# Kernel tuning notes

Measured on AMD Instinct MI355X. Metric: run time of the kernel, lower is better.

Reference implementation:

```python
import jax, jax.numpy as jnp
import numpy as np

HEADS, DIM_HEAD, LANDMARKS, PINV_ITERS = 8, 64, 256, 6
CONV_K = 33  # nystrom residual depthwise conv kernel


def _pinv(x, iters):
    # Moore-Penrose iterative pseudo-inverse (lucidrains nystrom-attention)
    ax = jnp.abs(x)
    denom = ax.sum(-1).max() * ax.sum(-2).max()
    z = jnp.swapaxes(x, -1, -2) / denom
    I = jnp.eye(x.shape[-1], dtype=x.dtype)
    for _ in range(iters):
        xz = x @ z
        z = 0.25 * z @ (13.0 * I - xz @ (15.0 * I - xz @ (7.0 * I - xz)))
    return z


def _nystrom(x, qkv_w, out_w, out_b, conv_w):
    b, n, _ = x.shape
    m = LANDMARKS
    pad = (m - n % m) % m
    x = jnp.pad(x, ((0, 0), (pad, 0), (0, 0)))  # pad at front, as in reference impl
    npad = n + pad
    qkv = x @ qkv_w  # (b, npad, 3*h*dh), no bias
    q, k, v = jnp.split(qkv, 3, axis=-1)
    heads = lambda t: t.reshape(b, npad, HEADS, DIM_HEAD).transpose(0, 2, 1, 3)  # bhnd
    q, k, v = heads(q), heads(k), heads(v)
    q = q * (DIM_HEAD ** -0.5)
    l = npad // m
    q_l = q.reshape(b, HEADS, m, l, DIM_HEAD).mean(3)  # (b,h,m,dh) landmarks
    k_l = k.reshape(b, HEADS, m, l, DIM_HEAD).mean(3)
    attn1 = jax.nn.softmax(jnp.einsum('bhid,bhjd->bhij', q, k_l), -1)    # (b,h,npad,m)
    attn2 = jax.nn.softmax(jnp.einsum('bhid,bhjd->bhij', q_l, k_l), -1)  # (b,h,m,m)
    attn3 = jax.nn.softmax(jnp.einsum('bhid,bhjd->bhij', q_l, k), -1)    # (b,h,m,npad)
    out = (attn1 @ _pinv(attn2, PINV_ITERS)) @ (attn3 @ v)               # (b,h,npad,dh)
    # residual depthwise conv along sequence dim (groups=heads)
    res = jax.lax.conv_general_dilated(
        v, conv_w, (1, 1), ((CONV_K // 2, CONV_K // 2), (0, 0)),
        dimension_numbers=('NCHW', 'OIHW', 'NCHW'), feature_group_count=HEADS)
    out = out + res
    out = out.transpose(0, 2, 1, 3).reshape(b, npad, HEADS * DIM_HEAD)
    out = out @ out_w + out_b
    return out[:, -n:]  # drop front padding


def setup_inputs() -> dict:
    key = jax.random.key(0)
    ks = jax.random.split(key, 12)
    N, D, E, WP = 30000, 1024, 480000, 256
    inner = HEADS * DIM_HEAD
    s = lambda k, shape, fan: jax.random.normal(k, shape, jnp.float32) * (fan ** -0.5)
    return {
        'dense': jax.random.normal(ks[0], (1, N, D), jnp.float32),
        'edge_index': jax.random.randint(ks[1], (2, E), 0, N),
        'adj_vals': jax.random.uniform(ks[2], (E,), jnp.float32),
        'qkv_w': s(ks[3], (D, 3 * inner), D),
        'out_w': s(ks[4], (inner, D), inner),
        'out_b': jnp.zeros((D,), jnp.float32),
        'conv_w': s(ks[5], (HEADS, 1, CONV_K, 1), CONV_K),
        'wq_w': s(ks[6], (D, WP), D),
        'wq_b': jnp.zeros((WP,), jnp.float32),
        'wk_w': s(ks[7], (D, WP), D),
        'wk_b': jnp.zeros((WP,), jnp.float32),
        'wv_w': s(ks[8], (D, D), D),
        'wv_b': jnp.zeros((D,), jnp.float32),
    }


def reference(dense, edge_index, adj_vals, qkv_w, out_w, out_b, conv_w,
              wq_w, wq_b, wk_w, wk_b, wv_w, wv_b):
    n = dense.shape[1]
    enc = _nystrom(dense, qkv_w, out_w, out_b, conv_w)  # (1, n, D)
    encoder_output = enc[0] + dense                     # (1, n, D), broadcast as in torch
    x = encoder_output[0]                               # (n, D)
    # CustomAttention: per-edge dot-product scores
    q = x @ wq_w + wq_b                                 # (n, 256)
    k = x @ wk_w + wk_b
    scores = jnp.sum(q[edge_index[0]] * k[edge_index[1]], axis=-1) / jnp.sqrt(jnp.float32(q.shape[-1]))
    # NeighborAggregator: elementwise sparse mult by adjacency values, row-sum, global softmax
    A_raw = jax.ops.segment_sum(scores * adj_vals, edge_index[0], num_segments=n)  # (n,)
    norm_alpha = jax.nn.softmax(A_raw)
    value = dense @ wv_w + wv_b                         # (1, n, D)
    xl = norm_alpha[:, None] * value                    # (1, n, D)
    sw = jax.nn.sigmoid(-xl) ** 2
    xo = xl * 2.0 * sw + 2.0 * encoder_output * (1.0 - sw)
    return xo, A_raw
```

## Files before the change

kernel.cpp:

```cpp
#include <hip/hip_runtime.h>

#define NSEQ   30000
#define NPAD   30208
#define FPAD   208
#define DMODEL 1024
#define NHEAD  8
#define DHEAD  64
#define LM     256
#define LCHUNK 118
#define INNER  512
#define NCHUNK 59

typedef long long ll;
typedef unsigned short us;
typedef unsigned int uint32;
typedef __attribute__((ext_vector_type(8))) __bf16 bf16x8;
typedef __attribute__((ext_vector_type(4))) float f32x4;

__device__ __forceinline__ float b2f(us u) {
    union { unsigned int i; float f; } x; x.i = ((unsigned int)u) << 16; return x.f;
}
__device__ __forceinline__ us f2b(float f) {
    union { float f; unsigned int i; } x; x.f = f;
    unsigned int r = x.i + 0x7fffu + ((x.i >> 16) & 1u);
    return (us)(r >> 16);
}
__device__ __forceinline__ void gload16(const us* g, us* l) {
    __builtin_amdgcn_global_load_lds(
        (__attribute__((address_space(1))) void*)(const_cast<us*>(g)),
        (__attribute__((address_space(3))) void*)l, 16, 0, 0);
}

template<int EPI>
__global__ __launch_bounds__(256)
void bgemm(const us* __restrict__ A, const us* __restrict__ Bt,
           float* __restrict__ C, us* __restrict__ C2,
           const float* __restrict__ bias, const float* __restrict__ addp,
           int Mm, int Nn, int Kk, int lda, int ldb, int ldc, int ldadd,
           int Mstore, int Nstore, int rSub)
{
    __shared__ us As[2][128 * 32];
    __shared__ us Bs[2][128 * 32];

    int nwg = gridDim.x * gridDim.y;
    int orig = blockIdx.y * gridDim.x + blockIdx.x;
    int qd = nwg >> 3, rm = nwg & 7;
    int xcd = orig & 7, off = orig >> 3;
    int swz = (xcd < rm ? xcd * (qd + 1) : rm * (qd + 1) + (xcd - rm) * qd) + off;
    int by = swz / gridDim.x, bx = swz - by * gridDim.x;
    int m0 = by * 128, n0 = bx * 128;

    int tid = threadIdx.x, w = tid >> 6, lane = tid & 63;
    int wr = w >> 1, wc = w & 1;
    int nkt = Kk >> 5;

    int q0 = w * 128;
    int qa0 = q0 + lane, qa1 = q0 + 64 + lane;
    int r0s = qa0 >> 2, c0s = (qa0 & 3) ^ ((r0s >> 1) & 3);
    int r1s = qa1 >> 2, c1s = (qa1 & 3) ^ ((r1s >> 1) & 3);
    int ar0 = m0 + r0s; if (ar0 > Mm - 1) ar0 = Mm - 1;
    int ar1 = m0 + r1s; if (ar1 > Mm - 1) ar1 = Mm - 1;
    int br0 = n0 + r0s; if (br0 > Nn - 1) br0 = Nn - 1;
    int br1 = n0 + r1s; if (br1 > Nn - 1) br1 = Nn - 1;
    const us* pa0 = A + (ll)ar0 * lda + c0s * 8;
    const us* pa1 = A + (ll)ar1 * lda + c1s * 8;
    const us* pb0 = Bt + (ll)br0 * ldb + c0s * 8;
    const us* pb1 = Bt + (ll)br1 * ldb + c1s * 8;
    int la0o = q0 * 8, la1o = (q0 + 64) * 8;

    int l15 = lane & 15, l4 = lane >> 4;
    int aoff[4], boff[4];
#pragma unroll
    for (int f = 0; f < 4; f++) {
        int row = wr * 64 + f * 16 + l15;
        aoff[f] = row * 32 + ((l4 ^ ((row >> 1) & 3)) << 3);
        int col = wc * 64 + f * 16 + l15;
        boff[f] = col * 32 + ((l4 ^ ((col >> 1) & 3)) << 3);
    }

    f32x4 acc[4][4];
#pragma unroll
    for (int i = 0; i < 4; i++)
#pragma unroll
        for (int j = 0; j < 4; j++) acc[i][j] = (f32x4){0.f, 0.f, 0.f, 0.f};

    auto stage = [&](int buf, int kt) {
        int k0 = kt << 5;
        gload16(pa0 + k0, &As[buf][la0o]);
        gload16(pa1 + k0, &As[buf][la1o]);
        gload16(pb0 + k0, &Bs[buf][la0o]);
        gload16(pb1 + k0, &Bs[buf][la1o]);
    };

    stage(0, 0);
    for (int kt = 0; kt < nkt; ++kt) {
        int cur = kt & 1;
        if (kt + 1 < nkt) {
            stage(cur ^ 1, kt + 1);
            asm volatile("s_waitcnt vmcnt(4)" ::: "memory");
        } else {
            asm volatile("s_waitcnt vmcnt(0)" ::: "memory");
        }
        __builtin_amdgcn_s_barrier();
        asm volatile("" ::: "memory");
        bf16x8 af[4], bfr[4];
#pragma unroll
        for (int f = 0; f < 4; f++) af[f] = *(const bf16x8*)&As[cur][aoff[f]];
#pragma unroll
        for (int f = 0; f < 4; f++) bfr[f] = *(const bf16x8*)&Bs[cur][boff[f]];
#pragma unroll
        for (int i = 0; i < 4; i++)
#pragma unroll
            for (int j = 0; j < 4; j++)
                acc[i][j] = __builtin_amdgcn_mfma_f32_16x16x32_bf16(af[i], bfr[j], acc[i][j], 0, 0, 0);
        asm volatile("" ::: "memory");
        __builtin_amdgcn_s_barrier();
        asm volatile("" ::: "memory");
    }

#pragma unroll
    for (int fm = 0; fm < 4; fm++) {
        int rb = m0 + wr * 64 + fm * 16 + l4 * 4;
#pragma unroll
        for (int fn = 0; fn < 4; fn++) {
            int c = n0 + wc * 64 + fn * 16 + l15;
            if (c >= Nstore) continue;
#pragma unroll
            for (int i = 0; i < 4; i++) {
                int r = rb + i - rSub;
                if (r < 0 || r >= Mstore) continue;
                float v = acc[fm][fn][i];
                if (EPI == 3) {
                    int part = c >> 9, hh = (c >> 6) & 7, dd = c & 63;
                    float o = (part == 0) ? v * 0.125f : v;
                    C2[((ll)(part * 8 + hh) * NPAD + r) * 64 + dd] = f2b(o);
                } else if (EPI == 10) {
                    C2[(ll)r * ldc + c] = f2b(v + bias[c]);
                } else if (EPI == 12) {
                    C2[(ll)r * ldc + c] = f2b(v + bias[c] + addp[(ll)r * ldadd + c]);
                }
            }
        }
    }
}

__global__ __launch_bounds__(512)
void mega1(const us* __restrict__ XN, us* __restrict__ ZN, us* __restrict__ ZT,
           us* __restrict__ ZN2, us* __restrict__ ZT2,
           us* __restrict__ Y, us* __restrict__ W1T, us* __restrict__ W2T,
           us* __restrict__ W3T,
           const us* __restrict__ QLB, const us* __restrict__ Kh,
           const us* __restrict__ VT, us* __restrict__ KVPb, float* __restrict__ ZP,
           const us* __restrict__ Vh, const float* __restrict__ cw,
           us* __restrict__ ATTP,
           const us* __restrict__ DENSEP, const us* __restrict__ WVT,
           const float* __restrict__ wvb, us* __restrict__ VALB)
{
    __shared__ us LDSu[24576];
    int b = blockIdx.x;
    int tid = threadIdx.x, w = tid >> 6, lane = tid & 63;
    int l15 = lane & 15, l4 = lane >> 4;

    if (b < 8) {
        __builtin_amdgcn_s_setprio(1);
        ll hb = (ll)b << 16;
        int wr = w >> 2, wc = w & 3;
        int sra = tid >> 2, sca = ((tid & 3) ^ ((sra >> 1) & 3)) * 8;
        int q1 = tid + 512;
        int srb1 = q1 >> 2, scb1 = ((q1 & 3) ^ ((srb1 >> 1) & 3)) * 8;
        int aoff[4], boff[4];
#pragma unroll
        for (int f = 0; f < 4; f++) {
            int row = wr * 64 + f * 16 + l15;
            aoff[f] = row * 32 + ((l4 ^ ((row >> 1) & 3)) << 3);
            int col = wc * 64 + f * 16 + l15;
            boff[f] = 4096 + col * 32 + ((l4 ^ ((col >> 1) & 3)) << 3);
        }
        f32x4 acc[4][4];
        auto gemmS = [&](const us* Ah, const us* Bt) {
#pragma unroll
            for (int i = 0; i < 4; i++)
#pragma unroll
                for (int j = 0; j < 4; j++) acc[i][j] = (f32x4){0.f, 0.f, 0.f, 0.f};
            const us* pa  = Ah + (ll)sra * 256 + sca;
            const us* pb0 = Bt + (ll)sra * 256 + sca;
            const us* pb1 = Bt + (ll)srb1 * 256 + scb1;
            auto stg = [&](int buf, int kt) {
                int k0 = kt << 5;
                gload16(pa + k0, &LDSu[buf + tid * 8]);
                gload16(pb0 + k0, &LDSu[buf + 4096 + tid * 8]);
                gload16(pb1 + k0, &LDSu[buf + 8192 + tid * 8]);
            };
            stg(0, 0);
            for (int kt = 0; kt < 8; ++kt) {
                int buf = (kt & 1) * 12288;
                if (kt < 7) {
                    stg(buf ^ 12288, kt + 1);
                    asm volatile("s_waitcnt vmcnt(3)" ::: "memory");
                } else {
                    asm volatile("s_waitcnt vmcnt(0)" ::: "memory");
                }
                __builtin_amdgcn_s_barrier();
                asm volatile("" ::: "memory");
                bf16x8 af[4], bfr[4];
#pragma unroll
                for (int f = 0; f < 4; f++) af[f] = *(const bf16x8*)&LDSu[buf + aoff[f]];
#pragma unroll
                for (int f = 0; f < 4; f++) bfr[f] = *(const bf16x8*)&LDSu[buf + boff[f]];
#pragma unroll
                for (int i = 0; i < 4; i++)
#pragma unroll
                    for (int j = 0; j < 4; j++)
                        acc[i][j] = __builtin_amdgcn_mfma_f32_16x16x32_bf16(af[i], bfr[j], acc[i][j], 0, 0, 0);
                asm volatile("" ::: "memory");
                __builtin_amdgcn_s_barrier();
                asm volatile("" ::: "memory");
            }
        };

        us* znc = ZN; us* ztc = ZT; us* znn = ZN2; us* ztn = ZT2;
        for (int it = 0; it < 6; ++it) {
#pragma unroll
            for (int hf = 0; hf < 2; ++hf) {
                gemmS(XN + hb + hf * 32768, ztc + hb);
#pragma unroll
                for (int fm = 0; fm < 4; fm++) {
                    int rb = hf * 128 + wr * 64 + fm * 16 + l4 * 4;
#pragma unroll
                    for (int fn = 0; fn < 4; fn++) {
                        int c = wc * 64 + fn * 16 + l15;
                        ushort4 u;
#pragma unroll
                        for (int i = 0; i < 4; i++) {
                            float v = acc[fm][fn][i];
                            Y[hb + (ll)(rb + i) * 256 + c] = f2b(v);
                            ((us*)&u)[i] = f2b(((rb + i == c) ? 7.0f : 0.0f) - v);
                        }
                        *(ushort4*)&W1T[hb + (ll)c * 256 + rb] = u;
                    }
                }
            }
            __syncthreads();
#pragma unroll
            for (int hf = 0; hf < 2; ++hf) {
                gemmS(Y + hb + hf * 32768, W1T + hb);
#pragma unroll
                for (int fm = 0; fm < 4; fm++) {
                    int rb = hf * 128 + wr * 64 + fm * 16 + l4 * 4;
#pragma unroll
                    for (int fn = 0; fn < 4; fn++) {
                        int c = wc * 64 + fn * 16 + l15;
                        ushort4 u;
#pragma unroll
                        for (int i = 0; i < 4; i++)
                            ((us*)&u)[i] = f2b(((rb + i == c) ? 15.0f : 0.0f) - acc[fm][fn][i]);
                        *(ushort4*)&W2T[hb + (ll)c * 256 + rb] = u;
                    }
                }
            }
            __syncthreads();
#pragma unroll
            for (int hf = 0; hf < 2; ++hf) {
                gemmS(Y + hb + hf * 32768, W2T + hb);
#pragma unroll
                for (int fm = 0; fm < 4; fm++) {
                    int rb = hf * 128 + wr * 64 + fm * 16 + l4 * 4;
#pragma unroll
                    for (int fn = 0; fn < 4; fn++) {
                        int c = wc * 64 + fn * 16 + l15;
                        ushort4 u;
#pragma unroll
                        for (int i = 0; i < 4; i++)
                            ((us*)&u)[i] = f2b(((rb + i == c) ? 13.0f : 0.0f) - acc[fm][fn][i]);
                        *(ushort4*)&W3T[hb + (ll)c * 256 + rb] = u;
                    }
                }
            }
            __syncthreads();
#pragma unroll
            for (int hf = 0; hf < 2; ++hf) {
                gemmS(znc + hb + hf * 32768, W3T + hb);
#pragma unroll
                for (int fm = 0; fm < 4; fm++) {
                    int rb = hf * 128 + wr * 64 + fm * 16 + l4 * 4;
#pragma unroll
                    for (int fn = 0; fn < 4; fn++) {
                        int c = wc * 64 + fn * 16 + l15;
                        ushort4 u;
#pragma unroll
                        for (int i = 0; i < 4; i++) {
                            us q = f2b(0.25f * acc[fm][fn][i]);
                            znn[hb + (ll)(rb + i) * 256 + c] = q;
                            ((us*)&u)[i] = q;
                        }
                        *(ushort4*)&ztn[hb + (ll)c * 256 + rb] = u;
                    }
                }
            }
            __syncthreads();
            us* tp;
            tp = znc; znc = znn; znn = tp;
            tp = ztc; ztc = ztn; ztn = tp;
        }
    } else if (b < 480) {
        if (w >= 4) return;
        int idx = b - 8;
        int h = idx & 7, chunk = idx >> 3;
        int c0 = chunk * 512;
        const us* QLh = QLB + (ll)h * 16384;
        const us* Khh = Kh + (ll)h * NPAD * 64;
        const us* VTh = VT + (ll)h * 64 * NPAD;
        us* P = &LDSu[w * 4096];

        bf16x8 aq[4][2];
#pragma unroll
        for (int fm = 0; fm < 4; fm++)
#pragma unroll
            for (int ks = 0; ks < 2; ks++)
                aq[fm][ks] = *(const bf16x8*)&QLh[(w * 64 + fm * 16 + l15) * 64 + l4 * 8 + ks * 32];

        f32x4 acc2[4][4];
        float zacc[4][4];
#pragma unroll
        for (int a = 0; a < 4; a++)
#pragma unroll
            for (int bb = 0; bb < 4; bb++) { acc2[a][bb] = (f32x4){0.f,0.f,0.f,0.f}; zacc[a][bb] = 0.f; }

        for (int sub = 0; sub < 8; ++sub) {
            int s0 = c0 + sub * 64;
            f32x4 s[4][4];
#pragma unroll
            for (int a = 0; a < 4; a++)
#pragma unroll
                for (int bb = 0; bb < 4; bb++) s[a][bb] = (f32x4){0.f,0.f,0.f,0.f};
#pragma unroll
            for (int ks = 0; ks < 2; ks++) {
                bf16x8 bk[4];
#pragma unroll
                for (int fn = 0; fn < 4; fn++)
                    bk[fn] = *(const bf16x8*)&Khh[(ll)(s0 + fn * 16 + l15) * 64 + l4 * 8 + ks * 32];
#pragma unroll
                for (int fm = 0; fm < 4; fm++)
#pragma unroll
                    for (int fn = 0; fn < 4; fn++)
                        s[fm][fn] = __builtin_amdgcn_mfma_f32_16x16x32_bf16(aq[fm][ks], bk[fn], s[fm][fn], 0, 0, 0);
            }
#pragma unroll
            for (int fm = 0; fm < 4; fm++)
#pragma unroll
                for (int i = 0; i < 4; i++) {
                    int row = fm * 16 + l4 * 4 + i;
#pragma unroll
                    for (int fn = 0; fn < 4; fn++) {
                        float e = __expf(s[fm][fn][i]);
                        zacc[fm][i] += e;
                        int col = fn * 16 + l15;
                        P[row * 64 + (((col >> 3) ^ (row & 7)) << 3) + (col & 7)] = f2b(e);
                    }
                }
#pragma unroll
            for (int ks = 0; ks < 2; ks++) {
                bf16x8 ap[4], bv[4];
#pragma unroll
                for (int fm = 0; fm < 4; fm++) {
                    int row = fm * 16 + l15;
                    int ch = (l4 + ks * 4) ^ (row & 7);
                    ap[fm] = *(const bf16x8*)&P[row * 64 + ch * 8];
                }
#pragma unroll
                for (int fn = 0; fn < 4; fn++)
                    bv[fn] = *(const bf16x8*)&VTh[(ll)(fn * 16 + l15) * NPAD + s0 + l4 * 8 + ks * 32];
#pragma unroll
                for (int fm = 0; fm < 4; fm++)
#pragma unroll
                    for (int fn = 0; fn < 4; fn++)
                        acc2[fm][fn] = __builtin_amdgcn_mfma_f32_16x16x32_bf16(ap[fm], bv[fn], acc2[fm][fn], 0, 0, 0);
            }
        }
        us* KP = KVPb + ((ll)h * NCHUNK + chunk) * 16384;
#pragma unroll
        for (int fm = 0; fm < 4; fm++)
#pragma unroll
            for (int fn = 0; fn < 4; fn++)
#pragma unroll
                for (int i = 0; i < 4; i++)
                    KP[(w * 64 + fm * 16 + l4 * 4 + i) * 64 + fn * 16 + l15] = f2b(acc2[fm][fn][i]);
#pragma unroll
        for (int fm = 0; fm < 4; fm++)
#pragma unroll
            for (int i = 0; i < 4; i++) {
                float zz = zacc[fm][i];
                zz += __shfl_xor(zz, 1, 64); zz += __shfl_xor(zz, 2, 64);
                zz += __shfl_xor(zz, 4, 64); zz += __shfl_xor(zz, 8, 64);
                if (l15 == 0)
                    ZP[((ll)h * NCHUNK + chunk) * 256 + w * 64 + fm * 16 + l4 * 4 + i] = zz;
            }
    } else if (b < 2360) {
        int vb = b - 480;
        int bx = vb & 7, by = vb >> 3;
        int m0 = by * 128, n0 = bx * 128;
        int wr = w >> 2, wc = w & 3;
        int sra = tid >> 2, sca = ((tid & 3) ^ ((sra >> 1) & 3)) * 8;
        int grow = m0 + sra; if (grow > NSEQ - 1) grow = NSEQ - 1;
        const us* pa = DENSEP + (ll)(grow + FPAD) * 1024 + sca;
        const us* pb = WVT + (ll)(n0 + sra) * 1024 + sca;
        int aoff[4], boff[2];
#pragma unroll
        for (int f = 0; f < 4; f++) {
            int row = wr * 64 + f * 16 + l15;
            aoff[f] = row * 32 + ((l4 ^ ((row >> 1) & 3)) << 3);
        }
#pragma unroll
        for (int f = 0; f < 2; f++) {
            int col = wc * 32 + f * 16 + l15;
            boff[f] = 4096 + col * 32 + ((l4 ^ ((col >> 1) & 3)) << 3);
        }
        f32x4 acc[4][2];
#pragma unroll
        for (int i = 0; i < 4; i++)
#pragma unroll
            for (int j = 0; j < 2; j++) acc[i][j] = (f32x4){0.f, 0.f, 0.f, 0.f};

        auto stg = [&](int buf, int kt) {
            int k0 = kt << 5;
            gload16(pa + k0, &LDSu[buf + tid * 8]);
            gload16(pb + k0, &LDSu[buf + 4096 + tid * 8]);
        };
        stg(0, 0);
        for (int kt = 0; kt < 32; ++kt) {
            int buf = (kt & 1) << 13;
            if (kt < 31) {
                stg(buf ^ 8192, kt + 1);
                asm volatile("s_waitcnt vmcnt(2)" ::: "memory");
            } else {
                asm volatile("s_waitcnt vmcnt(0)" ::: "memory");
            }
            __builtin_amdgcn_s_barrier();
            asm volatile("" ::: "memory");
            bf16x8 af[4], bfr[2];
#pragma unroll
            for (int f = 0; f < 4; f++) af[f] = *(const bf16x8*)&LDSu[buf + aoff[f]];
#pragma unroll
            for (int f = 0; f < 2; f++) bfr[f] = *(const bf16x8*)&LDSu[buf + boff[f]];
#pragma unroll
            for (int i = 0; i < 4; i++)
#pragma unroll
                for (int j = 0; j < 2; j++)
                    acc[i][j] = __builtin_amdgcn_mfma_f32_16x16x32_bf16(af[i], bfr[j], acc[i][j], 0, 0, 0);
            asm volatile("" ::: "memory");
            __builtin_amdgcn_s_barrier();
            asm volatile("" ::: "memory");
        }
#pragma unroll
        for (int fm = 0; fm < 4; fm++) {
            int rb = m0 + wr * 64 + fm * 16 + l4 * 4;
#pragma unroll
            for (int fn = 0; fn < 2; fn++) {
                int c = n0 + wc * 32 + fn * 16 + l15;
                float bias = wvb[c];
#pragma unroll
                for (int i = 0; i < 4; i++) {
                    int r = rb + i;
                    if (r < NSEQ) VALB[(ll)r * 1024 + c] = f2b(acc[fm][fn][i] + bias);
                }
            }
        }
    } else {
        int cc = b - 2360;
        int h = cc & 7, ig = cc >> 3;
        int i = ig * 16 + w * 2 + (lane >> 5);
        int d0 = (lane & 31) * 2;
        if (i >= NSEQ) return;
        const us* Vh2 = Vh + (ll)h * NPAD * 64;
        int n0 = FPAD + i - 16;
        float s0 = 0.f, s1 = 0.f;
#pragma unroll
        for (int kk = 0; kk < 33; ++kk) {
            int n = n0 + kk;
            if (n < NPAD) {
                float wgt = cw[h * 33 + kk];
                uint32 v2 = *(const uint32*)&Vh2[(ll)n * 64 + d0];
                s0 = fmaf(wgt, b2f((us)(v2 & 0xffff)), s0);
                s1 = fmaf(wgt, b2f((us)(v2 >> 16)), s1);
            }
        }
        uint32 o = (uint32)f2b(s0) | ((uint32)f2b(s1) << 16);
        *(uint32*)&ATTP[(ll)i * INNER + h * 64 + d0] = o;
    }
}

#define BM 128
#define BN 64
#define BK 16
template<int TB, int EPI>
__global__ __launch_bounds__(256)
void gemm_k(const float* __restrict__ A, const float* __restrict__ B, float* __restrict__ C,
            int Mm, int Nn, int Kk, int lda, int ldb, int ldc,
            ll sA, ll sB, ll sC, float alpha, float diagv)
{
    __shared__ float As[BK][132];
    __shared__ float Bs[BK][68];
    int batch = blockIdx.z;
    A += (ll)batch * sA; B += (ll)batch * sB; C += (ll)batch * sC;
    int m0 = blockIdx.y * BM, n0 = blockIdx.x * BN;
    int tid = threadIdx.x, tx = tid & 15, ty = tid >> 4;
    int arow_t = tid >> 1, akh = (tid & 1) * 8;
    bool avalid = (m0 + arow_t < Mm);
    const float* Arow = A + (ll)(m0 + arow_t) * lda;
    float acc[8][4];
#pragma unroll
    for (int i = 0; i < 8; i++)
#pragma unroll
        for (int j = 0; j < 4; j++) acc[i][j] = 0.f;
    for (int kt = 0; kt < Kk / BK; ++kt) {
        int k0 = kt * BK;
        float4 av0 = make_float4(0, 0, 0, 0), av1 = av0;
        if (avalid) {
            av0 = *(const float4*)(Arow + k0 + akh);
            av1 = *(const float4*)(Arow + k0 + akh + 4);
        }
        float4 bv;
        if (TB == 0) bv = *(const float4*)(B + (ll)(k0 + (tid >> 4)) * ldb + n0 + (tid & 15) * 4);
        else         bv = *(const float4*)(B + (ll)(n0 + (tid >> 2)) * ldb + k0 + (tid & 3) * 4);
        __syncthreads();
        As[akh + 0][arow_t] = av0.x; As[akh + 1][arow_t] = av0.y;
        As[akh + 2][arow_t] = av0.z; As[akh + 3][arow_t] = av0.w;
        As[akh + 4][arow_t] = av1.x; As[akh + 5][arow_t] = av1.y;
        As[akh + 6][arow_t] = av1.z; As[akh + 7][arow_t] = av1.w;
        if (TB == 0) *(float4*)&Bs[tid >> 4][(tid & 15) * 4] = bv;
        else {
            int bk4 = (tid & 3) * 4, bn = tid >> 2;
            Bs[bk4 + 0][bn] = bv.x; Bs[bk4 + 1][bn] = bv.y;
            Bs[bk4 + 2][bn] = bv.z; Bs[bk4 + 3][bn] = bv.w;
        }
        __syncthreads();
#pragma unroll
        for (int kk = 0; kk < BK; kk++) {
            float ar[8], br[4];
            *(float4*)&ar[0] = *(const float4*)&As[kk][ty * 8];
            *(float4*)&ar[4] = *(const float4*)&As[kk][ty * 8 + 4];
            *(float4*)&br[0] = *(const float4*)&Bs[kk][tx * 4];
#pragma unroll
            for (int i = 0; i < 8; i++)
#pragma unroll
                for (int j = 0; j < 4; j++) acc[i][j] = fmaf(ar[i], br[j], acc[i][j]);
        }
    }
    int c0 = n0 + tx * 4;
#pragma unroll
    for (int i = 0; i < 8; i++) {
        int r = m0 + ty * 8 + i;
        if (r >= Mm) continue;
#pragma unroll
        for (int j = 0; j < 4; j++) {
            int c = c0 + j;
            if (c >= Nn) continue;
            if (EPI == 0) C[(ll)r * ldc + c] = alpha * acc[i][j];
        }
    }
}

__global__ void kv_reduce2(const us* __restrict__ KVPb, const float* __restrict__ ZP,
                           float* __restrict__ KV)
{
    int e = blockIdx.x * 256 + threadIdx.x;
    int h = e >> 14, r = (e >> 6) & 255;
    float s = 0.f, z = 0.f;
    for (int c = 0; c < NCHUNK; ++c) {
        s += b2f(KVPb[((ll)h * NCHUNK + c) * 16384 + (e & 16383)]);
        z += ZP[((ll)h * NCHUNK + c) * 256 + r];
    }
    KV[e] = s / z;
}

__global__ __launch_bounds__(256)
void attn1_fused(const us* __restrict__ Qh, const us* __restrict__ KLB,
                 const us* __restrict__ PWT, us* __restrict__ ATTP)
{
    __shared__ us sP[4][4096];
    int h = blockIdx.y, r0 = blockIdx.x * 128;
    int w = threadIdx.x >> 6, lane = threadIdx.x & 63;
    int l15 = lane & 15, l4 = lane >> 4;
    const us* Qhh = Qh + (ll)h * NPAD * 64;
    const us* KLh = KLB + (ll)h * 16384;
    const us* PWh = PWT + (ll)h * 16384;
    us* P = sP[w];

    bf16x8 aq[2][2];
#pragma unroll
    for (int fm = 0; fm < 2; fm++)
#pragma unroll
        for (int ks = 0; ks < 2; ks++) {
            int r = r0 + w * 32 + fm * 16 + l15;
            if (r > NSEQ - 1) r = NSEQ - 1;
            aq[fm][ks] = *(const bf16x8*)&Qhh[(ll)(r + FPAD) * 64 + l4 * 8 + ks * 32];
        }

    f32x4 s[2][16];
#pragma unroll
    for (int a = 0; a < 2; a++)
#pragma unroll
        for (int bq = 0; bq < 16; bq++) s[a][bq] = (f32x4){0.f,0.f,0.f,0.f};
#pragma unroll
    for (int ks = 0; ks < 2; ks++)
#pragma unroll
        for (int fn = 0; fn < 16; fn++) {
            bf16x8 bk = *(const bf16x8*)&KLh[(fn * 16 + l15) * 64 + l4 * 8 + ks * 32];
            s[0][fn] = __builtin_amdgcn_mfma_f32_16x16x32_bf16(aq[0][ks], bk, s[0][fn], 0, 0, 0);
            s[1][fn] = __builtin_amdgcn_mfma_f32_16x16x32_bf16(aq[1][ks], bk, s[1][fn], 0, 0, 0);
        }
#pragma unroll
    for (int fm = 0; fm < 2; fm++)
#pragma unroll
        for (int i = 0; i < 4; i++) {
            float m = s[fm][0][i];
#pragma unroll
            for (int fn = 1; fn < 16; fn++) m = fmaxf(m, s[fm][fn][i]);
            m = fmaxf(m, __shfl_xor(m, 1, 64)); m = fmaxf(m, __shfl_xor(m, 2, 64));
            m = fmaxf(m, __shfl_xor(m, 4, 64)); m = fmaxf(m, __shfl_xor(m, 8, 64));
            float sum = 0.f;
#pragma unroll
            for (int fn = 0; fn < 16; fn++) {
                float e = __expf(s[fm][fn][i] - m);
                s[fm][fn][i] = e; sum += e;
            }
            sum += __shfl_xor(sum, 1, 64); sum += __shfl_xor(sum, 2, 64);
            sum += __shfl_xor(sum, 4, 64); sum += __shfl_xor(sum, 8, 64);
            float rinv = 1.0f / sum;
#pragma unroll
            for (int fn = 0; fn < 16; fn++) s[fm][fn][i] *= rinv;
        }
    f32x4 acc2[2][4];
#pragma unroll
    for (int a = 0; a < 2; a++)
#pragma unroll
        for (int bq = 0; bq < 4; bq++) acc2[a][bq] = (f32x4){0.f,0.f,0.f,0.f};
#pragma unroll
    for (int half = 0; half < 2; ++half) {
#pragma unroll
        for (int fm = 0; fm < 2; fm++)
#pragma unroll
            for (int i = 0; i < 4; i++) {
                int row = fm * 16 + l4 * 4 + i;
#pragma unroll
                for (int fh = 0; fh < 8; fh++) {
                    int col = fh * 16 + l15;
                    P[row * 128 + (((col >> 3) ^ (row & 7)) << 3) + (col & 7)] =
                        f2b(s[fm][half * 8 + fh][i]);
                }
            }
#pragma unroll
        for (int ks = 0; ks < 4; ks++) {
            bf16x8 ap[2];
#pragma unroll
            for (int fm = 0; fm < 2; fm++) {
                int row = fm * 16 + l15;
                int ch = (l4 + ks * 4) ^ (row & 7);
                ap[fm] = *(const bf16x8*)&P[row * 128 + ch * 8];
            }
#pragma unroll
            for (int fn = 0; fn < 4; fn++) {
                bf16x8 bp = *(const bf16x8*)&PWh[(ll)(fn * 16 + l15) * 256 + half * 128 + l4 * 8 + ks * 32];
                acc2[0][fn] = __builtin_amdgcn_mfma_f32_16x16x32_bf16(ap[0], bp, acc2[0][fn], 0, 0, 0);
                acc2[1][fn] = __builtin_amdgcn_mfma_f32_16x16x32_bf16(ap[1], bp, acc2[1][fn], 0, 0, 0);
            }
        }
    }
#pragma unroll
    for (int fm = 0; fm < 2; fm++)
#pragma unroll
        for (int fn = 0; fn < 4; fn++)
#pragma unroll
            for (int i = 0; i < 4; i++) {
                int r = r0 + w * 32 + fm * 16 + l4 * 4 + i;
                if (r < NSEQ) {
                    ll idx = (ll)r * 512 + h * 64 + fn * 16 + l15;
                    float a = acc2[fm][fn][i] + b2f(ATTP[idx]);
                    ATTP[idx] = f2b(a);
                }
            }
}

__global__ void trans_f2b(const float* __restrict__ in, us* __restrict__ out,
                          int R, int Cc, ll sI, ll sO)
{
    __shared__ float tile[32][33];
    const float* inp = in + (ll)blockIdx.z * sI;
    us* outp = out + (ll)blockIdx.z * sO;
    int r0 = blockIdx.y * 32, c0 = blockIdx.x * 32;
    int tx = threadIdx.x & 31, ty = threadIdx.x >> 5;
#pragma unroll
    for (int i = 0; i < 4; i++) {
        int r = r0 + ty + i * 8, c = c0 + tx;
        tile[ty + i * 8][tx] = (r < R && c < Cc) ? inp[(ll)r * Cc + c] : 0.f;
    }
    __syncthreads();
#pragma unroll
    for (int i = 0; i < 4; i++) {
        int c = c0 + ty + i * 8, r = r0 + tx;
        if (c < Cc && r < R) outp[(ll)c * R + r] = f2b(tile[tx][ty + i * 8]);
    }
}

__global__ void trans_b2b(const us* __restrict__ in, us* __restrict__ out,
                          int R, int Cc, ll sI, ll sO)
{
    __shared__ us tile[32][34];
    const us* inp = in + (ll)blockIdx.z * sI;
    us* outp = out + (ll)blockIdx.z * sO;
    int r0 = blockIdx.y * 32, c0 = blockIdx.x * 32;
    int tx = threadIdx.x & 31, ty = threadIdx.x >> 5;
#pragma unroll
    for (int i = 0; i < 4; i++) {
        int r = r0 + ty + i * 8, c = c0 + tx;
        tile[ty + i * 8][tx] = (r < R && c < Cc) ? inp[(ll)r * Cc + c] : (us)0;
    }
    __syncthreads();
#pragma unroll
    for (int i = 0; i < 4; i++) {
        int c = c0 + ty + i * 8, r = r0 + tx;
        if (c < Cc && r < R) outp[(ll)c * R + r] = tile[tx][ty + i * 8];
    }
}

__global__ void dense_pad_b(const float* __restrict__ x, us* __restrict__ o)
{
    ll e4 = ((ll)blockIdx.x * 256 + threadIdx.x) * 4;
    int r = (int)(e4 >> 10), c = (int)(e4 & 1023);
    ushort4 u;
    if (r < FPAD) { u.x = u.y = u.z = u.w = 0; }
    else {
        float4 v = *(const float4*)&x[(ll)(r - FPAD) * 1024 + c];
        u.x = f2b(v.x); u.y = f2b(v.y); u.z = f2b(v.z); u.w = f2b(v.w);
    }
    *(ushort4*)&o[e4] = u;
}

__global__ void concat_bias(const float* __restrict__ a, const float* __restrict__ b,
                            float* __restrict__ o)
{
    int t = threadIdx.x;
    o[t] = a[t]; o[256 + t] = b[t];
}

__global__ void landmark_mean_b(const us* __restrict__ src, float* __restrict__ dst,
                                us* __restrict__ dstb)
{
    int b = blockIdx.x;
    int h = b >> 8, jm = b & 255;
    int d = threadIdx.x;
    const us* p = src + ((ll)h * NPAD + (ll)jm * LCHUNK) * DHEAD + d;
    float s = 0.f;
    for (int jl = 0; jl < LCHUNK; ++jl) s += b2f(p[jl * DHEAD]);
    float v = s * (1.0f / LCHUNK);
    dst[((h << 8) + jm) * DHEAD + d] = v;
    dstb[((h << 8) + jm) * DHEAD + d] = f2b(v);
}

__global__ void rowsoftmax256(float* __restrict__ X)
{
    __shared__ float red[256];
    float* p = X + (ll)blockIdx.x * 256;
    int t = threadIdx.x;
    float v = p[t];
    red[t] = v; __syncthreads();
    for (int s = 128; s > 0; s >>= 1) { if (t < s) red[t] = fmaxf(red[t], red[t + s]); __syncthreads(); }
    float m = red[0]; __syncthreads();
    float e = expf(v - m);
    red[t] = e; __syncthreads();
    for (int s = 128; s > 0; s >>= 1) { if (t < s) red[t] += red[t + s]; __syncthreads(); }
    p[t] = e / red[0];
}

__global__ void colrow_max(const float* __restrict__ A2, float* __restrict__ hm)
{
    __shared__ float red[256];
    int h = blockIdx.x, t = threadIdx.x;
    const float* X = A2 + (ll)h * LM * LM;
    float cs = 0.f;
    for (int i = 0; i < LM; ++i) cs += X[i * LM + t];
    red[t] = cs; __syncthreads();
    for (int s = 128; s > 0; s >>= 1) { if (t < s) red[t] = fmaxf(red[t], red[t + s]); __syncthreads(); }
    if (t == 0) hm[h] = red[0];
    __syncthreads();
    float rs = 0.f;
    const float* Xr = X + (ll)t * LM;
    for (int j = 0; j < LM; ++j) rs += Xr[j];
    red[t] = rs; __syncthreads();
    for (int s = 128; s > 0; s >>= 1) { if (t < s) red[t] = fmaxf(red[t], red[t + s]); __syncthreads(); }
    if (t == 0) hm[8 + h] = red[0];
}

__global__ void denom_fin(const float* __restrict__ hm, float* __restrict__ scal)
{
    float cm = hm[0], rm = hm[8];
    for (int h = 1; h < 8; ++h) { cm = fmaxf(cm, hm[h]); rm = fmaxf(rm, hm[8 + h]); }
    scal[0] = 1.0f / (cm * rm);
}

__global__ void pinv_init(const float* __restrict__ A2, const float* __restrict__ scal,
                          us* __restrict__ XN, us* __restrict__ ZN, us* __restrict__ ZT)
{
    ll e = (ll)blockIdx.x * 256 + threadIdx.x;
    int h = (int)(e >> 16), r = (int)(e >> 8) & 255, c = (int)e & 255;
    float v = A2[e];
    XN[e] = f2b(v);
    float vs = v * scal[0];
    ZT[e] = f2b(vs);
    ZN[((ll)h << 16) + ((ll)c << 8) + r] = f2b(vs);
}

__global__ void zwiden(const us* __restrict__ zn, float* __restrict__ zf)
{
    ll e = (ll)blockIdx.x * 256 + threadIdx.x;
    zf[e] = b2f(zn[e]);
}

__global__ void zero_f32(float* __restrict__ p, int n)
{
    int i = blockIdx.x * 256 + threadIdx.x;
    if (i < n) p[i] = 0.f;
}

__global__ void edge_scores_b(const int* __restrict__ ei, const float* __restrict__ adj,
                              const us* __restrict__ qk2, float* __restrict__ Araw, int E)
{
    int gw = (blockIdx.x * 256 + threadIdx.x) >> 6;
    int lane = threadIdx.x & 63;
    if (gw >= E) return;
    int src = ei[gw], dst = ei[E + gw];
    const uint32* qp = (const uint32*)(qk2 + (ll)src * 512);
    const uint32* kp = (const uint32*)(qk2 + (ll)dst * 512 + 256);
    float acc = 0.f;
#pragma unroll
    for (int t = 0; t < 2; t++) {
        uint32 qu = qp[lane + t * 64], ku = kp[lane + t * 64];
        acc += b2f((us)(qu & 0xffff)) * b2f((us)(ku & 0xffff));
        acc += b2f((us)(qu >> 16)) * b2f((us)(ku >> 16));
    }
#pragma unroll
    for (int m = 32; m >= 1; m >>= 1) acc += __shfl_xor(acc, m, 64);
    if (lane == 0) atomicAdd(Araw + src, acc * adj[gw] * 0.0625f);
}

__global__ void softmax30k_stats(const float* __restrict__ A, float* __restrict__ scal)
{
    __shared__ float red[1024];
    int t = threadIdx.x;
    float m = -3.0e38f;
    for (int i = t; i < NSEQ; i += 1024) m = fmaxf(m, A[i]);
    red[t] = m; __syncthreads();
    for (int s = 512; s > 0; s >>= 1) { if (t < s) red[t] = fmaxf(red[t], red[t + s]); __syncthreads(); }
    m = red[0]; __syncthreads();
    float sum = 0.f;
    for (int i = t; i < NSEQ; i += 1024) sum += expf(A[i] - m);
    red[t] = sum; __syncthreads();
    for (int s = 512; s > 0; s >>= 1) { if (t < s) red[t] += red[t + s]; __syncthreads(); }
    if (t == 0) { scal[1] = m; scal[2] = red[0]; }
}

__global__ void alpha_kernel(const float* __restrict__ A, const float* __restrict__ scal,
                             float* __restrict__ alpha)
{
    int i = blockIdx.x * 256 + threadIdx.x;
    if (i < NSEQ) alpha[i] = expf(A[i] - scal[1]) / scal[2];
}

__global__ void gate_kernel(const float* __restrict__ alpha, const us* __restrict__ VALB,
                            const us* __restrict__ ENCB, float* __restrict__ OUT)
{
    ll e4 = ((ll)blockIdx.x * 256 + threadIdx.x) * 4;
    int i = (int)(e4 >> 10);
    float a = alpha[i];
    ushort4 vv = *(const ushort4*)&VALB[e4];
    ushort4 ee = *(const ushort4*)&ENCB[e4];
    float4 o;
    float* op = &o.x;
    const us* vp = (const us*)&vv;
    const us* ep = (const us*)&ee;
#pragma unroll
    for (int j = 0; j < 4; j++) {
        float xl = a * b2f(vp[j]);
        float sg = 1.0f / (1.0f + __expf(xl));
        float sw = sg * sg;
        op[j] = xl * 2.0f * sw + 2.0f * b2f(ep[j]) * (1.0f - sw);
    }
    *(float4*)&OUT[e4] = o;
}

extern "C" void kernel_launch(void* const* d_in, const int* in_sizes, int n_in,
                              void* d_out, int out_size, void* d_ws, size_t ws_size,
                              hipStream_t stream)
{
    const float* dense  = (const float*)d_in[0];
    const int*   ei     = (const int*)d_in[1];
    const float* adj    = (const float*)d_in[2];
    const float* qkv_w  = (const float*)d_in[3];
    const float* out_w  = (const float*)d_in[4];
    const float* out_b  = (const float*)d_in[5];
    const float* conv_w = (const float*)d_in[6];
    const float* wq_w   = (const float*)d_in[7];
    const float* wq_b   = (const float*)d_in[8];
    const float* wk_w   = (const float*)d_in[9];
    const float* wk_b   = (const float*)d_in[10];
    const float* wv_w   = (const float*)d_in[11];
    const float* wv_b   = (const float*)d_in[12];
    int E = in_sizes[2];

    char* w = (char*)d_ws;
    auto alloc = [&](ll bytes) { char* p = w; w += (bytes + 255) & ~(ll)255; return p; };

    us*    DENSEP = (us*)alloc((ll)NPAD * 1024 * 2);
    us*    QKVH   = (us*)alloc((ll)3 * 8 * NPAD * 64 * 2);
    us*    ENCB   = QKVH;
    us*    Qh = QKVH, *Kh = QKVH + (ll)8 * NPAD * 64, *Vh = QKVH + (ll)16 * NPAD * 64;
    us*    VT     = (us*)alloc((ll)8 * 64 * NPAD * 2);
    us*    QKVWT  = (us*)alloc((ll)1536 * 1024 * 2);
    us*    OUTWT  = (us*)alloc((ll)1024 * 512 * 2);
    us*    WQKT   = (us*)alloc((ll)512 * 1024 * 2);
    us*    WVT    = (us*)alloc((ll)1024 * 1024 * 2);
    float* WQKB   = (float*)alloc(512 * 4);
    float* QL     = (float*)alloc((ll)8 * 256 * 64 * 4);
    float* KL     = (float*)alloc((ll)8 * 256 * 64 * 4);
    us*    QLB    = (us*)alloc((ll)8 * 256 * 64 * 2);
    us*    KLB    = (us*)alloc((ll)8 * 256 * 64 * 2);
    float* A2     = (float*)alloc((ll)8 * 65536 * 4);
    us*    XN     = (us*)alloc((ll)8 * 65536 * 2);
    us*    ZN     = (us*)alloc((ll)8 * 65536 * 2);
    us*    ZT     = (us*)alloc((ll)8 * 65536 * 2);
    us*    ZN2    = (us*)alloc((ll)8 * 65536 * 2);
    us*    ZT2    = (us*)alloc((ll)8 * 65536 * 2);
    us*    Ybuf   = (us*)alloc((ll)8 * 65536 * 2);
    us*    W1T    = (us*)alloc((ll)8 * 65536 * 2);
    us*    W2T    = (us*)alloc((ll)8 * 65536 * 2);
    us*    W3T    = (us*)alloc((ll)8 * 65536 * 2);
    float* ZF     = (float*)alloc((ll)8 * 65536 * 4);
    us*    KVPb   = (us*)alloc((ll)8 * NCHUNK * 16384 * 2);
    float* ZP     = (float*)alloc((ll)8 * NCHUNK * 256 * 4);
    float* KV     = (float*)alloc((ll)8 * 16384 * 4);
    float* PW     = (float*)alloc((ll)8 * 16384 * 4);
    us*    PWT    = (us*)alloc((ll)8 * 16384 * 2);
    float* HM     = (float*)alloc(64 * 4);
    float* SC     = (float*)alloc(64 * 4);
    float* ALPHA  = (float*)alloc(30000 * 4);
    us*    ATTP   = (us*)alloc((ll)NSEQ * 512 * 2);
    us*    QK2B   = ATTP;
    us*    VALB   = (us*)alloc((ll)NSEQ * 1024 * 2);

    float* OUT  = (float*)d_out;
    float* ARAW = OUT + (ll)NSEQ * DMODEL;

    trans_f2b<<<dim3(48, 32, 1), 256, 0, stream>>>(qkv_w, QKVWT, 1024, 1536, 0, 0);
    trans_f2b<<<dim3(32, 16, 1), 256, 0, stream>>>(out_w, OUTWT, 512, 1024, 0, 0);
    trans_f2b<<<dim3(8, 32, 1), 256, 0, stream>>>(wq_w, WQKT, 1024, 256, 0, 0);
    trans_f2b<<<dim3(8, 32, 1), 256, 0, stream>>>(wk_w, WQKT + (ll)256 * 1024, 1024, 256, 0, 0);
    trans_f2b<<<dim3(32, 32, 1), 256, 0, stream>>>(wv_w, WVT, 1024, 1024, 0, 0);
    concat_bias<<<1, 256, 0, stream>>>(wq_b, wk_b, WQKB);
    dense_pad_b<<<NPAD, 256, 0, stream>>>(dense, DENSEP);

    bgemm<3><<<dim3(12, 236, 1), 256, 0, stream>>>(DENSEP, QKVWT, nullptr, QKVH,
        nullptr, nullptr, NPAD, 1536, 1024, 1024, 1024, 0, 0, NPAD, 1536, 0);

    landmark_mean_b<<<2048, 64, 0, stream>>>(Qh, QL, QLB);
    landmark_mean_b<<<2048, 64, 0, stream>>>(Kh, KL, KLB);

    gemm_k<1, 0><<<dim3(4, 2, 8), 256, 0, stream>>>(QL, KL, A2, LM, LM, DHEAD,
        DHEAD, DHEAD, LM, LM * DHEAD, LM * DHEAD, LM * LM, 1.f, 0.f);
    rowsoftmax256<<<2048, 256, 0, stream>>>(A2);
    colrow_max<<<8, 256, 0, stream>>>(A2, HM);
    denom_fin<<<1, 1, 0, stream>>>(HM, SC);
    pinv_init<<<2048, 256, 0, stream>>>(A2, SC, XN, ZN, ZT);

    trans_b2b<<<dim3(2, 944, 8), 256, 0, stream>>>(Vh, VT, NPAD, 64, (ll)NPAD * 64, (ll)64 * NPAD);

    mega1<<<17360, 512, 0, stream>>>(XN, ZN, ZT, ZN2, ZT2, Ybuf, W1T, W2T, W3T,
                                     QLB, Kh, VT, KVPb, ZP, Vh, conv_w, ATTP,
                                     DENSEP, WVT, wv_b, VALB);

    kv_reduce2<<<512, 256, 0, stream>>>(KVPb, ZP, KV);

    zwiden<<<2048, 256, 0, stream>>>(ZN, ZF);
    gemm_k<0, 0><<<dim3(1, 2, 8), 256, 0, stream>>>(ZF, KV, PW, LM, DHEAD, LM,
        LM, DHEAD, DHEAD, 65536, 16384, 16384, 1.f, 0.f);
    trans_f2b<<<dim3(2, 8, 8), 256, 0, stream>>>(PW, PWT, 256, 64, 16384, 16384);

    attn1_fused<<<dim3(235, 8), 256, 0, stream>>>(Qh, KLB, PWT, ATTP);

    bgemm<12><<<dim3(8, 235, 1), 256, 0, stream>>>(ATTP, OUTWT, nullptr, ENCB,
        out_b, dense, NSEQ, 1024, 512, 512, 512, 1024, 1024, NSEQ, 1024, 0);

    bgemm<10><<<dim3(4, 235, 1), 256, 0, stream>>>(ENCB, WQKT, nullptr, QK2B,
        WQKB, nullptr, NSEQ, 512, 1024, 1024, 1024, 512, 0, NSEQ, 512, 0);

    zero_f32<<<(NSEQ + 255) / 256, 256, 0, stream>>>(ARAW, NSEQ);
    edge_scores_b<<<(E + 3) / 4, 256, 0, stream>>>(ei, adj, QK2B, ARAW, E);
    softmax30k_stats<<<1, 1024, 0, stream>>>(ARAW, SC);
    alpha_kernel<<<(NSEQ + 255) / 256, 256, 0, stream>>>(ARAW, SC, ALPHA);

    gate_kernel<<<30000, 256, 0, stream>>>(ALPHA, VALB, ENCB, OUT);
}
```

Baseline: 1.435 ms.

## Move attn1 softmax into mega kernel and fuse pinv-KV product

Computes the attn1 score GEMM and softmax for all query rows as extra block ranges inside the mega kernel. This lets that work overlap with the pinv and other phases, and the result is written to a new bf16 buffer P1. A later kernel then only performs the P·PW product from P1. The widen, f32 GEMM and transpose chain for PW is replaced by a single fused bf16 MFMA kernel. The cost is about 120MB of extra P1 global writes and reads.

```diff
diff --git a/kernel.cpp b/kernel.cpp
--- a/kernel.cpp
+++ b/kernel.cpp
@@ -154,7 +154,9 @@
            const us* __restrict__ Vh, const float* __restrict__ cw,
            us* __restrict__ ATTP,
            const us* __restrict__ DENSEP, const us* __restrict__ WVT,
-           const float* __restrict__ wvb, us* __restrict__ VALB)
+           const float* __restrict__ wvb, us* __restrict__ VALB,
+           const us* __restrict__ Qh, const us* __restrict__ KLB,
+           us* __restrict__ P1)
 {
     __shared__ us LDSu[24576];
     int b = blockIdx.x;
@@ -465,8 +467,58 @@
                 }
             }
         }
+    } else if (b < 4248) {
+        int idx = b - 2360;
+        int h = idx & 7, rc = idx >> 3;
+        int rb0 = rc * 128 + w * 16;
+        const us* Qhh = Qh + (ll)h * NPAD * 64;
+        const us* KLh = KLB + (ll)h * 16384;
+        us* P1h = P1 + (ll)h * NPAD * 256;
+
+        int ra = rb0 + l15; if (ra > NSEQ - 1) ra = NSEQ - 1;
+        bf16x8 aq0 = *(const bf16x8*)&Qhh[(ll)(ra + FPAD) * 64 + l4 * 8];
+        bf16x8 aq1 = *(const bf16x8*)&Qhh[(ll)(ra + FPAD) * 64 + l4 * 8 + 32];
+
+        f32x4 s[16];
+#pragma unroll
+        for (int fn = 0; fn < 16; fn++) s[fn] = (f32x4){0.f,0.f,0.f,0.f};
+#pragma unroll
+        for (int fn = 0; fn < 16; fn++) {
+            bf16x8 bk0 = *(const bf16x8*)&KLh[(fn * 16 + l15) * 64 + l4 * 8];
+            bf16x8 bk1 = *(const bf16x8*)&KLh[(fn * 16 + l15) * 64 + l4 * 8 + 32];
+            s[fn] = __builtin_amdgcn_mfma_f32_16x16x32_bf16(aq0, bk0, s[fn], 0, 0, 0);
+            s[fn] = __builtin_amdgcn_mfma_f32_16x16x32_bf16(aq1, bk1, s[fn], 0, 0, 0);
+        }
+#pragma unroll
+        for (int i = 0; i < 4; i++) {
+            float m = s[0][i];
+#pragma unroll
+            for (int fn = 1; fn < 16; fn++) m = fmaxf(m, s[fn][i]);
+            m = fmaxf(m, __shfl_xor(m, 1, 64)); m = fmaxf(m, __shfl_xor(m, 2, 64));
+            m = fmaxf(m, __shfl_xor(m, 4, 64)); m = fmaxf(m, __shfl_xor(m, 8, 64));
+            float sum = 0.f;
+#pragma unroll
+            for (int fn = 0; fn < 16; fn++) {
+                float e = __expf(s[fn][i] - m);
+                s[fn][i] = e; sum += e;
+            }
+            sum += __shfl_xor(sum, 1, 64); sum += __shfl_xor(sum, 2, 64);
+            sum += __shfl_xor(sum, 4, 64); sum += __shfl_xor(sum, 8, 64);
+            float rinv = 1.0f / sum;
+#pragma unroll
+            for (int fn = 0; fn < 16; fn++) s[fn][i] *= rinv;
+        }
+#pragma unroll
+        for (int i = 0; i < 4; i++) {
+            int r = rb0 + l4 * 4 + i;
+            if (r < NSEQ) {
+#pragma unroll
+                for (int fn = 0; fn < 16; fn++)
+                    P1h[(ll)r * 256 + fn * 16 + l15] = f2b(s[fn][i]);
+            }
+        }
     } else {
-        int cc = b - 2360;
+        int cc = b - 4248;
         int h = cc & 7, ig = cc >> 3;
         int i = ig * 16 + w * 2 + (lane >> 5);
         int d0 = (lane & 31) * 2;
@@ -574,96 +626,89 @@
 }
 
 __global__ __launch_bounds__(256)
-void attn1_fused(const us* __restrict__ Qh, const us* __restrict__ KLB,
-                 const us* __restrict__ PWT, us* __restrict__ ATTP)
-{
-    __shared__ us sP[4][4096];
+void pw_fused(const us* __restrict__ ZN, const float* __restrict__ KV,
+              us* __restrict__ PWT)
+{
+    __shared__ us KT[64 * 264];
+    int h = blockIdx.x;
+    int tid = threadIdx.x, w = tid >> 6, lane = tid & 63;
+    int l15 = lane & 15, l4 = lane >> 4;
+    const float* KVh = KV + (ll)h * 16384;
+#pragma unroll
+    for (int i = 0; i < 64; ++i) {
+        int idx = i * 256 + tid;
+        int r = idx >> 6, c = idx & 63;
+        KT[c * 264 + r] = f2b(KVh[idx]);
+    }
+    __syncthreads();
+    const us* Zh = ZN + ((ll)h << 16);
+    f32x4 acc[4][4];
+#pragma unroll
+    for (int i = 0; i < 4; i++)
+#pragma unroll
+        for (int j = 0; j < 4; j++) acc[i][j] = (f32x4){0.f, 0.f, 0.f, 0.f};
+    int rw = w * 64;
+    for (int ks = 0; ks < 8; ++ks) {
+        int k0 = ks * 32 + l4 * 8;
+        bf16x8 af[4], bfr[4];
+#pragma unroll
+        for (int f = 0; f < 4; f++)
+            af[f] = *(const bf16x8*)&Zh[(ll)(rw + f * 16 + l15) * 256 + k0];
+#pragma unroll
+        for (int f = 0; f < 4; f++)
+            bfr[f] = *(const bf16x8*)&KT[(f * 16 + l15) * 264 + k0];
+#pragma unroll
+        for (int i = 0; i < 4; i++)
+#pragma unroll
+            for (int j = 0; j < 4; j++)
+                acc[i][j] = __builtin_amdgcn_mfma_f32_16x16x32_bf16(af[i], bfr[j], acc[i][j], 0, 0, 0);
+    }
+    us* PWh = PWT + (ll)h * 16384;
+#pragma unroll
+    for (int fm = 0; fm < 4; fm++)
+#pragma unroll
+        for (int fn = 0; fn < 4; fn++)
+#pragma unroll
+            for (int i = 0; i < 4; i++) {
+                int r = rw + fm * 16 + l4 * 4 + i;
+                int c = fn * 16 + l15;
+                PWh[c * 256 + r] = f2b(acc[fm][fn][i]);
+            }
+}
+
+__global__ __launch_bounds__(256)
+void attn1_pv(const us* __restrict__ P1, const us* __restrict__ PWT,
+              us* __restrict__ ATTP)
+{
     int h = blockIdx.y, r0 = blockIdx.x * 128;
     int w = threadIdx.x >> 6, lane = threadIdx.x & 63;
     int l15 = lane & 15, l4 = lane >> 4;
-    const us* Qhh = Qh + (ll)h * NPAD * 64;
-    const us* KLh = KLB + (ll)h * 16384;
+    const us* P1h = P1 + (ll)h * NPAD * 256;
     const us* PWh = PWT + (ll)h * 16384;
-    us* P = sP[w];
-
-    bf16x8 aq[2][2];
-#pragma unroll
-    for (int fm = 0; fm < 2; fm++)
-#pragma unroll
-        for (int ks = 0; ks < 2; ks++) {
-            int r = r0 + w * 32 + fm * 16 + l15;
-            if (r > NSEQ - 1) r = NSEQ - 1;
-            aq[fm][ks] = *(const bf16x8*)&Qhh[(ll)(r + FPAD) * 64 + l4 * 8 + ks * 32];
-        }
-
-    f32x4 s[2][16];
+
+    int ra[2];
+#pragma unroll
+    for (int fm = 0; fm < 2; fm++) {
+        int r = r0 + w * 32 + fm * 16 + l15;
+        ra[fm] = (r > NSEQ - 1) ? (NSEQ - 1) : r;
+    }
+    f32x4 acc[2][4];
 #pragma unroll
     for (int a = 0; a < 2; a++)
 #pragma unroll
-        for (int bq = 0; bq < 16; bq++) s[a][bq] = (f32x4){0.f,0.f,0.f,0.f};
-#pragma unroll
-    for (int ks = 0; ks < 2; ks++)
-#pragma unroll
-        for (int fn = 0; fn < 16; fn++) {
-            bf16x8 bk = *(const bf16x8*)&KLh[(fn * 16 + l15) * 64 + l4 * 8 + ks * 32];
-            s[0][fn] = __builtin_amdgcn_mfma_f32_16x16x32_bf16(aq[0][ks], bk, s[0][fn], 0, 0, 0);
-            s[1][fn] = __builtin_amdgcn_mfma_f32_16x16x32_bf16(aq[1][ks], bk, s[1][fn], 0, 0, 0);
-        }
-#pragma unroll
-    for (int fm = 0; fm < 2; fm++)
-#pragma unroll
-        for (int i = 0; i < 4; i++) {
-            float m = s[fm][0][i];
-#pragma unroll
-            for (int fn = 1; fn < 16; fn++) m = fmaxf(m, s[fm][fn][i]);
-            m = fmaxf(m, __shfl_xor(m, 1, 64)); m = fmaxf(m, __shfl_xor(m, 2, 64));
-            m = fmaxf(m, __shfl_xor(m, 4, 64)); m = fmaxf(m, __shfl_xor(m, 8, 64));
-            float sum = 0.f;
-#pragma unroll
-            for (int fn = 0; fn < 16; fn++) {
-                float e = __expf(s[fm][fn][i] - m);
-                s[fm][fn][i] = e; sum += e;
-            }
-            sum += __shfl_xor(sum, 1, 64); sum += __shfl_xor(sum, 2, 64);
-            sum += __shfl_xor(sum, 4, 64); sum += __shfl_xor(sum, 8, 64);
-            float rinv = 1.0f / sum;
-#pragma unroll
-            for (int fn = 0; fn < 16; fn++) s[fm][fn][i] *= rinv;
-        }
-    f32x4 acc2[2][4];
-#pragma unroll
-    for (int a = 0; a < 2; a++)
-#pragma unroll
-        for (int bq = 0; bq < 4; bq++) acc2[a][bq] = (f32x4){0.f,0.f,0.f,0.f};
-#pragma unroll
-    for (int half = 0; half < 2; ++half) {
+        for (int bq = 0; bq < 4; bq++) acc[a][bq] = (f32x4){0.f,0.f,0.f,0.f};
+
+#pragma unroll
+    for (int ks = 0; ks < 8; ++ks) {
+        bf16x8 ap[2];
 #pragma unroll
         for (int fm = 0; fm < 2; fm++)
-#pragma unroll
-            for (int i = 0; i < 4; i++) {
-                int row = fm * 16 + l4 * 4 + i;
-#pragma unroll
-                for (int fh = 0; fh < 8; fh++) {
-                    int col = fh * 16 + l15;
-                    P[row * 128 + (((col >> 3) ^ (row & 7)) << 3) + (col & 7)] =
-                        f2b(s[fm][half * 8 + fh][i]);
-                }
-            }
-#pragma unroll
-        for (int ks = 0; ks < 4; ks++) {
-            bf16x8 ap[2];
-#pragma unroll
-            for (int fm = 0; fm < 2; fm++) {
-                int row = fm * 16 + l15;
-                int ch = (l4 + ks * 4) ^ (row & 7);
-                ap[fm] = *(const bf16x8*)&P[row * 128 + ch * 8];
-            }
-#pragma unroll
-            for (int fn = 0; fn < 4; fn++) {
-                bf16x8 bp = *(const bf16x8*)&PWh[(ll)(fn * 16 + l15) * 256 + half * 128 + l4 * 8 + ks * 32];
-                acc2[0][fn] = __builtin_amdgcn_mfma_f32_16x16x32_bf16(ap[0], bp, acc2[0][fn], 0, 0, 0);
-                acc2[1][fn] = __builtin_amdgcn_mfma_f32_16x16x32_bf16(ap[1], bp, acc2[1][fn], 0, 0, 0);
-            }
+            ap[fm] = *(const bf16x8*)&P1h[(ll)ra[fm] * 256 + ks * 32 + l4 * 8];
+#pragma unroll
+        for (int fn = 0; fn < 4; fn++) {
+            bf16x8 bp = *(const bf16x8*)&PWh[(fn * 16 + l15) * 256 + ks * 32 + l4 * 8];
+            acc[0][fn] = __builtin_amdgcn_mfma_f32_16x16x32_bf16(ap[0], bp, acc[0][fn], 0, 0, 0);
+            acc[1][fn] = __builtin_amdgcn_mfma_f32_16x16x32_bf16(ap[1], bp, acc[1][fn], 0, 0, 0);
         }
     }
 #pragma unroll
@@ -675,7 +720,7 @@
                 int r = r0 + w * 32 + fm * 16 + l4 * 4 + i;
                 if (r < NSEQ) {
                     ll idx = (ll)r * 512 + h * 64 + fn * 16 + l15;
-                    float a = acc2[fm][fn][i] + b2f(ATTP[idx]);
+                    float a = acc[fm][fn][i] + b2f(ATTP[idx]);
                     ATTP[idx] = f2b(a);
                 }
             }
@@ -808,12 +853,6 @@
     float vs = v * scal[0];
     ZT[e] = f2b(vs);
     ZN[((ll)h << 16) + ((ll)c << 8) + r] = f2b(vs);
-}
-
-__global__ void zwiden(const us* __restrict__ zn, float* __restrict__ zf)
-{
-    ll e = (ll)blockIdx.x * 256 + threadIdx.x;
-    zf[e] = b2f(zn[e]);
 }
 
 __global__ void zero_f32(float* __restrict__ p, int n)
@@ -934,11 +973,9 @@
     us*    W1T    = (us*)alloc((ll)8 * 65536 * 2);
     us*    W2T    = (us*)alloc((ll)8 * 65536 * 2);
     us*    W3T    = (us*)alloc((ll)8 * 65536 * 2);
-    float* ZF     = (float*)alloc((ll)8 * 65536 * 4);
     us*    KVPb   = (us*)alloc((ll)8 * NCHUNK * 16384 * 2);
     float* ZP     = (float*)alloc((ll)8 * NCHUNK * 256 * 4);
     float* KV     = (float*)alloc((ll)8 * 16384 * 4);
-    float* PW     = (float*)alloc((ll)8 * 16384 * 4);
     us*    PWT    = (us*)alloc((ll)8 * 16384 * 2);
     float* HM     = (float*)alloc(64 * 4);
     float* SC     = (float*)alloc(64 * 4);
@@ -946,6 +983,7 @@
     us*    ATTP   = (us*)alloc((ll)NSEQ * 512 * 2);
     us*    QK2B   = ATTP;
     us*    VALB   = (us*)alloc((ll)NSEQ * 1024 * 2);
+    us*    P1     = (us*)alloc((ll)8 * NPAD * 256 * 2);
 
     float* OUT  = (float*)d_out;
     float* ARAW = OUT + (ll)NSEQ * DMODEL;
@@ -973,18 +1011,14 @@
 
     trans_b2b<<<dim3(2, 944, 8), 256, 0, stream>>>(Vh, VT, NPAD, 64, (ll)NPAD * 64, (ll)64 * NPAD);
 
-    mega1<<<17360, 512, 0, stream>>>(XN, ZN, ZT, ZN2, ZT2, Ybuf, W1T, W2T, W3T,
+    mega1<<<19248, 512, 0, stream>>>(XN, ZN, ZT, ZN2, ZT2, Ybuf, W1T, W2T, W3T,
                                      QLB, Kh, VT, KVPb, ZP, Vh, conv_w, ATTP,
-                                     DENSEP, WVT, wv_b, VALB);
+                                     DENSEP, WVT, wv_b, VALB, Qh, KLB, P1);
 
     kv_reduce2<<<512, 256, 0, stream>>>(KVPb, ZP, KV);
-
-    zwiden<<<2048, 256, 0, stream>>>(ZN, ZF);
-    gemm_k<0, 0><<<dim3(1, 2, 8), 256, 0, stream>>>(ZF, KV, PW, LM, DHEAD, LM,
-        LM, DHEAD, DHEAD, 65536, 16384, 16384, 1.f, 0.f);
-    trans_f2b<<<dim3(2, 8, 8), 256, 0, stream>>>(PW, PWT, 256, 64, 16384, 16384);
-
-    attn1_fused<<<dim3(235, 8), 256, 0, stream>>>(Qh, KLB, PWT, ATTP);
+    pw_fused<<<8, 256, 0, stream>>>(ZN, KV, PWT);
+
+    attn1_pv<<<dim3(235, 8), 256, 0, stream>>>(P1, PWT, ATTP);
 
     bgemm<12><<<dim3(8, 235, 1), 256, 0, stream>>>(ATTP, OUTWT, nullptr, ENCB,
         out_b, dense, NSEQ, 1024, 512, 512, 512, 1024, 1024, NSEQ, 1024, 0);
```

Result: faster. 1.352 ms (-5.8%).
